# Kernel tuning notes

Hardware: AMD Instinct MI355X
Metric: run time of the kernel (lower is better)

## Reference

```python
import jax, jax.numpy as jnp
import numpy as np


def setup_inputs() -> dict:
    key = jax.random.key(0)
    k1, k2, k3, k4, k5 = jax.random.split(key, 5)
    B, Q, M, P, C = 32, 256, 128, 64, 20
    return {
        "pred_logits": jax.random.normal(k1, (B, Q, C + 1), dtype=jnp.float32),
        "pred_polylines": jax.random.normal(k2, (B, Q, P, 2), dtype=jnp.float32),
        "target_polylines": jax.random.normal(k3, (B, M, P, 2), dtype=jnp.float32),
        "src_idx": jax.random.randint(k4, (B, M), 0, Q),
        "labels": jax.random.randint(k5, (B, M), 0, C),
    }


def reference(pred_logits, pred_polylines, target_polylines, src_idx, labels):
    B, Q, C1 = pred_logits.shape
    num_classes = C1 - 1
    M = src_idx.shape[1]
    num_polylines = jnp.maximum(jnp.float32(B * M), 1.0)
    batch_ix = jnp.arange(B)[:, None]  # [B,1]

    # ---- classification loss (cross entropy, unmatched queries -> no-object class) ----
    target_classes = jnp.full((B, Q), num_classes, dtype=jnp.int32)
    target_classes = target_classes.at[batch_ix, src_idx].set(labels.astype(jnp.int32))
    logp = jax.nn.log_softmax(pred_logits, axis=-1)  # [B,Q,C+1]
    loss_ce = -jnp.take_along_axis(logp, target_classes[..., None], axis=-1).mean()

    # ---- polyline loss: symmetric chamfer-style mean of min L1 distances ----
    src_poly = pred_polylines[batch_ix, src_idx]  # [B,M,P,2]
    # all-pairs L1 distance matrix per matched pair: [B,M,P,P]
    dist = jnp.abs(src_poly[:, :, :, None, :] - target_polylines[:, :, None, :, :]).sum(-1)
    min1 = dist.min(axis=2).mean(axis=-1)  # min over src points, mean over tgt points: [B,M]
    min2 = dist.min(axis=3).mean(axis=-1)  # min over tgt points, mean over src points: [B,M]
    loss_polyline = ((min1 + min2) * 0.5).sum() / num_polylines

    # ---- direction loss: 1 - cosine(start->end vectors) ----
    eps = 1e-6
    sd = src_poly[:, :, -1] - src_poly[:, :, 0]  # [B,M,2]
    td = target_polylines[:, :, -1] - target_polylines[:, :, 0]
    sd = sd / (jnp.linalg.norm(sd, axis=-1, keepdims=True) + eps)
    td = td / (jnp.linalg.norm(td, axis=-1, keepdims=True) + eps)
    cos = (sd * td).sum(-1)  # [B,M]
    loss_direction = (1.0 - cos).sum() / num_polylines

    return jnp.stack([loss_ce, loss_polyline, loss_direction])
```

## Files before the change

### kernel.cpp

```cpp
#include <hip/hip_runtime.h>
#include <math.h>

constexpr int kB = 32;
constexpr int kQ = 256;
constexpr int kM = 128;
constexpr int kP = 64;
constexpr int kC = 20;
constexpr int kC1 = kC + 1;

constexpr int kPairsPerBlock = 16;
constexpr int kPolyBlocks   = (kB * kM) / kPairsPerBlock;
constexpr int kCeBlocks     = kB;
constexpr int kWsPoly = 0;
constexpr int kWsDir  = 1024;
constexpr int kWsCe   = 2048;

__global__ __launch_bounds__(256) void partial_kernel(const float* __restrict__ logits,
                                                      const float2* __restrict__ pred_poly,
                                                      const float2* __restrict__ tgt_poly,
                                                      const int* __restrict__ src_idx,
                                                      const int* __restrict__ labels,
                                                      float* __restrict__ ws) {
    const int tid  = threadIdx.x;
    const int lane = tid & 63;
    const int w    = tid >> 6;

    if (blockIdx.x < kPolyBlocks) {
        __shared__ float2 s_src[kPairsPerBlock][kP];
        __shared__ float2 s_tgt[kPairsPerBlock][kP];
        __shared__ int    s_sidx[kPairsPerBlock];

        const int base = blockIdx.x * kPairsPerBlock;
        const int b    = base >> 7;

        if (tid < kPairsPerBlock) s_sidx[tid] = src_idx[base + tid];
        __syncthreads();

        #pragma unroll
        for (int i = 0; i < 8; ++i) {
            const int g      = i * 256 + tid;
            const int p      = g >> 7;
            const int within = g & 127;
            if (within < kP) {
                s_src[p][within] = pred_poly[(size_t)(b * kQ + s_sidx[p]) * kP + within];
            } else {
                s_tgt[p][within - kP] = tgt_poly[(size_t)(base + p) * kP + (within - kP)];
            }
        }
        __syncthreads();

        float accPoly = 0.f, accDir = 0.f;
        #pragma unroll
        for (int i = 0; i < 4; ++i) {
            const int p = w * 4 + i;
            const float2 ms = s_src[p][lane];
            const float2 mt = s_tgt[p][lane];
            float minJ = 1e30f, minI = 1e30f;
            #pragma unroll 8
            for (int j = 0; j < kP; ++j) {
                const float2 sj = s_src[p][j];
                const float2 tj = s_tgt[p][j];
                minJ = fminf(minJ, fabsf(ms.x - tj.x) + fabsf(ms.y - tj.y));
                minI = fminf(minI, fabsf(sj.x - mt.x) + fabsf(sj.y - mt.y));
            }
            float val = minI + minJ;
            #pragma unroll
            for (int off = 32; off > 0; off >>= 1) val += __shfl_down(val, off, 64);
            if (lane == 0) {
                accPoly += val;
                const float2 s0 = s_src[p][0], s1 = s_src[p][kP - 1];
                const float2 t0 = s_tgt[p][0], t1 = s_tgt[p][kP - 1];
                const float sdx = s1.x - s0.x, sdy = s1.y - s0.y;
                const float tdx = t1.x - t0.x, tdy = t1.y - t0.y;
                const float sn = sqrtf(sdx * sdx + sdy * sdy) + 1e-6f;
                const float tn = sqrtf(tdx * tdx + tdy * tdy) + 1e-6f;
                accDir += 1.0f - (sdx * tdx + sdy * tdy) / (sn * tn);
            }
        }
        if (lane == 0) {
            const int wid = blockIdx.x * 4 + w;
            ws[kWsPoly + wid] = accPoly;
            ws[kWsDir + wid]  = accDir;
        }
    } else {
        const int b = blockIdx.x - kPolyBlocks;
        const int q = tid;
        __shared__ int c_idx[kM];
        __shared__ int c_lab[kM];
        if (tid < kM) {
            c_idx[tid] = src_idx[b * kM + tid];
            c_lab[tid] = labels[b * kM + tid];
        }
        __syncthreads();

        int tc = kC;
        #pragma unroll 4
        for (int m = 0; m < kM; ++m) {
            if (c_idx[m] == q) tc = c_lab[m];
        }

        const float* lp = logits + (size_t)(b * kQ + q) * kC1;
        float v[kC1];
        float mx = -1e30f;
        #pragma unroll
        for (int c = 0; c < kC1; ++c) { v[c] = lp[c]; mx = fmaxf(mx, v[c]); }
        float se = 0.f;
        #pragma unroll
        for (int c = 0; c < kC1; ++c) se += __expf(v[c] - mx);
        float val = -(v[tc] - mx - __logf(se));

        #pragma unroll
        for (int off = 32; off > 0; off >>= 1) val += __shfl_down(val, off, 64);
        if (lane == 0) ws[kWsCe + b * 4 + w] = val;
    }
}

__global__ __launch_bounds__(256) void finalize_kernel(const float* __restrict__ ws,
                                                       float* __restrict__ out) {
    const int tid  = threadIdx.x;
    const int lane = tid & 63;
    const int w    = tid >> 6;

    float p = 0.f, d = 0.f, c = 0.f;
    #pragma unroll
    for (int k = 0; k < 4; ++k) {
        p += ws[kWsPoly + tid + 256 * k];
        d += ws[kWsDir + tid + 256 * k];
    }
    if (tid < 128) c = ws[kWsCe + tid];

    #pragma unroll
    for (int off = 32; off > 0; off >>= 1) {
        p += __shfl_down(p, off, 64);
        d += __shfl_down(d, off, 64);
        c += __shfl_down(c, off, 64);
    }

    __shared__ float sp[4], sd[4], sc[4];
    if (lane == 0) { sp[w] = p; sd[w] = d; sc[w] = c; }
    __syncthreads();
    if (tid == 0) {
        const float P = sp[0] + sp[1] + sp[2] + sp[3];
        const float D = sd[0] + sd[1] + sd[2] + sd[3];
        const float C = sc[0] + sc[1] + sc[2] + sc[3];
        out[0] = C * (1.0f / (float)(kB * kQ));
        out[1] = P * (0.5f / ((float)kP * (float)(kB * kM)));
        out[2] = D * (1.0f / (float)(kB * kM));
    }
}

extern "C" void kernel_launch(void* const* d_in, const int* in_sizes, int n_in,
                              void* d_out, int out_size, void* d_ws, size_t ws_size,
                              hipStream_t stream) {
    const float*  pred_logits = (const float*)d_in[0];
    const float2* pred_poly   = (const float2*)d_in[1];
    const float2* tgt_poly    = (const float2*)d_in[2];
    const int*    src_idx     = (const int*)d_in[3];
    const int*    labels      = (const int*)d_in[4];
    float* out = (float*)d_out;
    float* ws  = (float*)d_ws;

    partial_kernel<<<kPolyBlocks + kCeBlocks, 256, 0, stream>>>(
        pred_logits, pred_poly, tgt_poly, src_idx, labels, ws);
    finalize_kernel<<<1, 256, 0, stream>>>(ws, out);
}
```

Baseline: 73.13 us.

## Fuse finalize into main kernel via last-block atomic counter, spread CE work

Merges the partial and finalize kernels into one launch, where the last block to finish, found through an atomic counter, does the final reduction. The cross-entropy work moves from 32 dedicated blocks into the first wave of each of the 256 poly blocks, 32 queries per block. Global and shared polyline loads are widened to float4, and the inner loop handles two points per iteration. This removes one kernel launch and the CE tail blocks, but adds a memset launch and atomics.

```diff
diff --git a/kernel.cpp b/kernel.cpp
--- a/kernel.cpp
+++ b/kernel.cpp
@@ -9,125 +9,143 @@
 constexpr int kC1 = kC + 1;
 
 constexpr int kPairsPerBlock = 16;
-constexpr int kPolyBlocks   = (kB * kM) / kPairsPerBlock;
-constexpr int kCeBlocks     = kB;
+constexpr int kBlocks = (kB * kM) / kPairsPerBlock;
+
 constexpr int kWsPoly = 0;
 constexpr int kWsDir  = 1024;
 constexpr int kWsCe   = 2048;
+constexpr int kWsCnt  = 2304;
 
-__global__ __launch_bounds__(256) void partial_kernel(const float* __restrict__ logits,
-                                                      const float2* __restrict__ pred_poly,
-                                                      const float2* __restrict__ tgt_poly,
-                                                      const int* __restrict__ src_idx,
-                                                      const int* __restrict__ labels,
-                                                      float* __restrict__ ws) {
+__global__ __launch_bounds__(256) void fused_kernel(const float* __restrict__ logits,
+                                                    const float2* __restrict__ pred_poly,
+                                                    const float2* __restrict__ tgt_poly,
+                                                    const int* __restrict__ src_idx,
+                                                    const int* __restrict__ labels,
+                                                    float* __restrict__ ws,
+                                                    float* __restrict__ out) {
     const int tid  = threadIdx.x;
     const int lane = tid & 63;
     const int w    = tid >> 6;
+    const int bid  = blockIdx.x;
 
-    if (blockIdx.x < kPolyBlocks) {
-        __shared__ float2 s_src[kPairsPerBlock][kP];
-        __shared__ float2 s_tgt[kPairsPerBlock][kP];
-        __shared__ int    s_sidx[kPairsPerBlock];
+    __shared__ float2 s_src[kPairsPerBlock][kP];
+    __shared__ float2 s_tgt[kPairsPerBlock][kP];
+    __shared__ int    s_sidx[kPairsPerBlock];
+    __shared__ int    c_idx[kM];
+    __shared__ int    c_lab[kM];
+    __shared__ int    s_last;
+    __shared__ float  sp[4], sd[4], sc[4];
 
-        const int base = blockIdx.x * kPairsPerBlock;
-        const int b    = base >> 7;
+    const int base = bid * kPairsPerBlock;
+    const int b    = base >> 7;
 
-        if (tid < kPairsPerBlock) s_sidx[tid] = src_idx[base + tid];
-        __syncthreads();
+    if (tid < kPairsPerBlock) s_sidx[tid] = src_idx[base + tid];
+    if (tid < kM) {
+        c_idx[tid] = src_idx[b * kM + tid];
+        c_lab[tid] = labels[b * kM + tid];
+    }
+    __syncthreads();
 
-        #pragma unroll
-        for (int i = 0; i < 8; ++i) {
-            const int g      = i * 256 + tid;
-            const int p      = g >> 7;
-            const int within = g & 127;
-            if (within < kP) {
-                s_src[p][within] = pred_poly[(size_t)(b * kQ + s_sidx[p]) * kP + within];
-            } else {
-                s_tgt[p][within - kP] = tgt_poly[(size_t)(base + p) * kP + (within - kP)];
-            }
+    #pragma unroll
+    for (int i = 0; i < 4; ++i) {
+        const int g      = i * 256 + tid;
+        const int p      = g >> 6;
+        const int within = g & 63;
+        if (within < 32) {
+            const float4* s4 = reinterpret_cast<const float4*>(
+                pred_poly + (size_t)(b * kQ + s_sidx[p]) * kP);
+            reinterpret_cast<float4*>(s_src[p])[within] = s4[within];
+        } else {
+            const float4* t4 = reinterpret_cast<const float4*>(
+                tgt_poly + (size_t)(base + p) * kP);
+            reinterpret_cast<float4*>(s_tgt[p])[within - 32] = t4[within - 32];
         }
-        __syncthreads();
+    }
+    __syncthreads();
 
-        float accPoly = 0.f, accDir = 0.f;
-        #pragma unroll
-        for (int i = 0; i < 4; ++i) {
-            const int p = w * 4 + i;
-            const float2 ms = s_src[p][lane];
-            const float2 mt = s_tgt[p][lane];
-            float minJ = 1e30f, minI = 1e30f;
-            #pragma unroll 8
-            for (int j = 0; j < kP; ++j) {
-                const float2 sj = s_src[p][j];
-                const float2 tj = s_tgt[p][j];
-                minJ = fminf(minJ, fabsf(ms.x - tj.x) + fabsf(ms.y - tj.y));
-                minI = fminf(minI, fabsf(sj.x - mt.x) + fabsf(sj.y - mt.y));
-            }
-            float val = minI + minJ;
-            #pragma unroll
-            for (int off = 32; off > 0; off >>= 1) val += __shfl_down(val, off, 64);
-            if (lane == 0) {
-                accPoly += val;
-                const float2 s0 = s_src[p][0], s1 = s_src[p][kP - 1];
-                const float2 t0 = s_tgt[p][0], t1 = s_tgt[p][kP - 1];
-                const float sdx = s1.x - s0.x, sdy = s1.y - s0.y;
-                const float tdx = t1.x - t0.x, tdy = t1.y - t0.y;
-                const float sn = sqrtf(sdx * sdx + sdy * sdy) + 1e-6f;
-                const float tn = sqrtf(tdx * tdx + tdy * tdy) + 1e-6f;
-                accDir += 1.0f - (sdx * tdx + sdy * tdy) / (sn * tn);
-            }
+    float accPoly = 0.f, accDir = 0.f;
+    #pragma unroll
+    for (int i = 0; i < 4; ++i) {
+        const int p = w * 4 + i;
+        const float2 ms = s_src[p][lane];
+        const float2 mt = s_tgt[p][lane];
+        const float4* srow = reinterpret_cast<const float4*>(s_src[p]);
+        const float4* trow = reinterpret_cast<const float4*>(s_tgt[p]);
+        float minJ = 1e30f, minI = 1e30f;
+        #pragma unroll 8
+        for (int jj = 0; jj < kP / 2; ++jj) {
+            const float4 tj = trow[jj];
+            const float4 sj = srow[jj];
+            minJ = fminf(minJ, fminf(fabsf(ms.x - tj.x) + fabsf(ms.y - tj.y),
+                                     fabsf(ms.x - tj.z) + fabsf(ms.y - tj.w)));
+            minI = fminf(minI, fminf(fabsf(sj.x - mt.x) + fabsf(sj.y - mt.y),
+                                     fabsf(sj.z - mt.x) + fabsf(sj.w - mt.y)));
         }
-        if (lane == 0) {
-            const int wid = blockIdx.x * 4 + w;
-            ws[kWsPoly + wid] = accPoly;
-            ws[kWsDir + wid]  = accDir;
-        }
-    } else {
-        const int b = blockIdx.x - kPolyBlocks;
-        const int q = tid;
-        __shared__ int c_idx[kM];
-        __shared__ int c_lab[kM];
-        if (tid < kM) {
-            c_idx[tid] = src_idx[b * kM + tid];
-            c_lab[tid] = labels[b * kM + tid];
-        }
-        __syncthreads();
-
-        int tc = kC;
-        #pragma unroll 4
-        for (int m = 0; m < kM; ++m) {
-            if (c_idx[m] == q) tc = c_lab[m];
-        }
-
-        const float* lp = logits + (size_t)(b * kQ + q) * kC1;
-        float v[kC1];
-        float mx = -1e30f;
-        #pragma unroll
-        for (int c = 0; c < kC1; ++c) { v[c] = lp[c]; mx = fmaxf(mx, v[c]); }
-        float se = 0.f;
-        #pragma unroll
-        for (int c = 0; c < kC1; ++c) se += __expf(v[c] - mx);
-        float val = -(v[tc] - mx - __logf(se));
-
+        float val = minI + minJ;
         #pragma unroll
         for (int off = 32; off > 0; off >>= 1) val += __shfl_down(val, off, 64);
-        if (lane == 0) ws[kWsCe + b * 4 + w] = val;
+        if (lane == 0) {
+            accPoly += val;
+            const float2 s0 = s_src[p][0], s1 = s_src[p][kP - 1];
+            const float2 t0 = s_tgt[p][0], t1 = s_tgt[p][kP - 1];
+            const float sdx = s1.x - s0.x, sdy = s1.y - s0.y;
+            const float tdx = t1.x - t0.x, tdy = t1.y - t0.y;
+            const float sn = sqrtf(sdx * sdx + sdy * sdy) + 1e-6f;
+            const float tn = sqrtf(tdx * tdx + tdy * tdy) + 1e-6f;
+            accDir += 1.0f - (sdx * tdx + sdy * tdy) / (sn * tn);
+        }
     }
-}
+    if (lane == 0) {
+        const int wid = bid * 4 + w;
+        __hip_atomic_store(&ws[kWsPoly + wid], accPoly, __ATOMIC_RELAXED, __HIP_MEMORY_SCOPE_AGENT);
+        __hip_atomic_store(&ws[kWsDir + wid],  accDir,  __ATOMIC_RELAXED, __HIP_MEMORY_SCOPE_AGENT);
+    }
 
-__global__ __launch_bounds__(256) void finalize_kernel(const float* __restrict__ ws,
-                                                       float* __restrict__ out) {
-    const int tid  = threadIdx.x;
-    const int lane = tid & 63;
-    const int w    = tid >> 6;
+    if (w == 0) {
+        float ceVal = 0.f;
+        if (lane < 32) {
+            const int q = ((bid & 7) << 5) + lane;
+            int tc = kC;
+            #pragma unroll 4
+            for (int m = 0; m < kM; ++m) {
+                if (c_idx[m] == q) tc = c_lab[m];
+            }
+            const float* lp = logits + (size_t)(b * kQ + q) * kC1;
+            float mx = -1e30f;
+            #pragma unroll
+            for (int c = 0; c < kC1; ++c) mx = fmaxf(mx, lp[c]);
+            float se = 0.f, vt = 0.f;
+            #pragma unroll
+            for (int c = 0; c < kC1; ++c) {
+                const float x = lp[c];
+                se += __expf(x - mx);
+                if (c == tc) vt = x;
+            }
+            ceVal = -(vt - mx - __logf(se));
+        }
+        #pragma unroll
+        for (int off = 32; off > 0; off >>= 1) ceVal += __shfl_down(ceVal, off, 64);
+        if (lane == 0)
+            __hip_atomic_store(&ws[kWsCe + bid], ceVal, __ATOMIC_RELAXED, __HIP_MEMORY_SCOPE_AGENT);
+    }
+
+    __syncthreads();
+    if (tid == 0) {
+        unsigned int* cnt = reinterpret_cast<unsigned int*>(ws + kWsCnt);
+        const unsigned int old =
+            __hip_atomic_fetch_add(cnt, 1u, __ATOMIC_ACQ_REL, __HIP_MEMORY_SCOPE_AGENT);
+        s_last = (old == (unsigned int)(kBlocks - 1));
+    }
+    __syncthreads();
+    if (!s_last) return;
 
     float p = 0.f, d = 0.f, c = 0.f;
     #pragma unroll
     for (int k = 0; k < 4; ++k) {
-        p += ws[kWsPoly + tid + 256 * k];
-        d += ws[kWsDir + tid + 256 * k];
+        p += __hip_atomic_load(&ws[kWsPoly + tid + 256 * k], __ATOMIC_RELAXED, __HIP_MEMORY_SCOPE_AGENT);
+        d += __hip_atomic_load(&ws[kWsDir  + tid + 256 * k], __ATOMIC_RELAXED, __HIP_MEMORY_SCOPE_AGENT);
     }
-    if (tid < 128) c = ws[kWsCe + tid];
+    c = __hip_atomic_load(&ws[kWsCe + tid], __ATOMIC_RELAXED, __HIP_MEMORY_SCOPE_AGENT);
 
     #pragma unroll
     for (int off = 32; off > 0; off >>= 1) {
@@ -136,7 +154,6 @@
         c += __shfl_down(c, off, 64);
     }
 
-    __shared__ float sp[4], sd[4], sc[4];
     if (lane == 0) { sp[w] = p; sd[w] = d; sc[w] = c; }
     __syncthreads();
     if (tid == 0) {
@@ -160,7 +177,8 @@
     float* out = (float*)d_out;
     float* ws  = (float*)d_ws;
 
-    partial_kernel<<<kPolyBlocks + kCeBlocks, 256, 0, stream>>>(
-        pred_logits, pred_poly, tgt_poly, src_idx, labels, ws);
-    finalize_kernel<<<1, 256, 0, stream>>>(ws, out);
+    hipMemsetAsync(ws + kWsCnt, 0, sizeof(unsigned int), stream);
+
+    fused_kernel<<<kBlocks, 256, 0, stream>>>(
+        pred_logits, pred_poly, tgt_poly, src_idx, labels, ws, out);
 }
```

After: 84.20 us. 1.15x slower.
